# Kernel optimization log

Hardware: AMD Instinct MI355X
Metric: run time of the kernel (lower is better)

The kernel has to match this reference:

```python
import jax, jax.numpy as jnp
import numpy as np

B, IN_F, OUT_F = 1024, 512, 512


def setup_inputs() -> dict:
    key = jax.random.key(0)
    k1, k2 = jax.random.split(key)
    x = jax.random.uniform(k1, (B, IN_F), dtype=jnp.float32)
    weight = jax.random.uniform(k2, (IN_F, OUT_F), dtype=jnp.float32)
    return {"x": x, "weight": weight}


def reference(x, weight):
    # Max-min fuzzy composition (tropical semiring 'matmul'):
    # out[b, o] = max_i min(x[b, i], W[i, o])
    # x: [B, IN], weight: [IN, OUT] -> out: [B, OUT]
    return jnp.max(jnp.minimum(x[:, :, None], weight[None, :, :]), axis=1)
```

## Files before the change

kernel.cpp:

```cpp
#include <hip/hip_runtime.h>


typedef unsigned int u32;
typedef u32 u32x2 __attribute__((ext_vector_type(2)));
typedef u32 u32x4 __attribute__((ext_vector_type(4)));
typedef float f4 __attribute__((ext_vector_type(4)));
typedef float f2 __attribute__((ext_vector_type(2)));
typedef __fp16 h2 __attribute__((ext_vector_type(2)));

#define IN_F 512
#define OUT_F 512
#define XS_BYTES 8192
#define WS_BYTES 8192
#define BUF_BYTES (XS_BYTES + WS_BYTES)

static __device__ __forceinline__ u32 pkcvt(float a, float b) {
  return __builtin_bit_cast(u32, __builtin_amdgcn_cvt_pkrtz(a, b));
}
static __device__ __forceinline__ u32 pkmin(u32 a, u32 b) {
  u32 d;
  asm("v_pk_min_u16 %0, %1, %2" : "=v"(d) : "v"(a), "v"(b));
  return d;
}
static __device__ __forceinline__ u32 pkmax(u32 a, u32 b) {
  u32 d;
  asm("v_pk_max_u16 %0, %1, %2" : "=v"(d) : "v"(a), "v"(b));
  return d;
}

__global__ __launch_bounds__(1024, 4) void maxmin_v3(const float* __restrict__ X,
                                                     const float* __restrict__ W,
                                                     float* __restrict__ Out) {
  __shared__ __align__(16) char smem[65536];

  const int tid  = threadIdx.x;
  const int wv   = tid >> 6;
  const int lane = tid & 63;
  const int ty   = lane >> 3;
  const int tx   = lane & 7;
  const int b0   = blockIdx.x * 32;
  const int o0   = blockIdx.y * 64;

  const int xrow = tid & 31;
  const int xq   = tid >> 5;
  const bool dox = (xq < 16);
  const float* xg = X + (b0 + xrow) * IN_F + xq * 4;

  const int wrow = tid >> 4;
  const int wc4  = tid & 15;
  const float* wg = W + wrow * OUT_F + o0 + wc4 * 4;

  const int xs_r = (wv * 4) * 128 + ty * 16;
  const int ws_r = XS_BYTES + (wv * 4) * 128 + tx * 16;

  const int xw = xrow * 4;
  const int ww = XS_BYTES + wrow * 128 + wc4 * 8;

  u32 acc[4][4] = {};

  auto stage = [&](char* buf, f4 xv, f4 wv4) {
    u32x2 wp = {pkcvt(wv4.x, wv4.y), pkcvt(wv4.z, wv4.w)};
    *(u32x2*)(buf + ww) = wp;
    if (dox) {
      *(u32*)(buf + (4 * xq + 0) * 128 + xw) = pkcvt(xv.x, xv.x);
      *(u32*)(buf + (4 * xq + 1) * 128 + xw) = pkcvt(xv.y, xv.y);
      *(u32*)(buf + (4 * xq + 2) * 128 + xw) = pkcvt(xv.z, xv.z);
      *(u32*)(buf + (4 * xq + 3) * 128 + xw) = pkcvt(xv.w, xv.w);
    }
  };

  f4 xv = {};
  if (dox) xv = *(const f4*)xg;
  f4 wv4 = *(const f4*)wg;
  stage(smem, xv, wv4);
  __syncthreads();

  for (int c = 0; c < 8; ++c) {
    f4 nx = {}, nw = {};
    if (c < 7) {
      if (dox) nx = *(const f4*)(xg + (c + 1) * 64);
      nw = *(const f4*)(wg + (c + 1) * 64 * OUT_F);
    }
    const char* buf = smem + (c & 1) * BUF_BYTES;
#pragma unroll
    for (int j = 0; j < 4; ++j) {
      u32x4 xqv = *(const u32x4*)(buf + xs_r + j * 128);
      u32x4 wqv = *(const u32x4*)(buf + ws_r + j * 128);
#pragma unroll
      for (int i = 0; i < 4; ++i)
#pragma unroll
        for (int jj = 0; jj < 4; ++jj)
          acc[i][jj] = pkmax(acc[i][jj], pkmin(xqv[i], wqv[jj]));
    }
    if (c < 7) stage(smem + ((c + 1) & 1) * BUF_BYTES, nx, nw);
    __syncthreads();
  }

#pragma unroll
  for (int i = 0; i < 4; ++i) {
    u32x4 v = {acc[i][0], acc[i][1], acc[i][2], acc[i][3]};
    *(u32x4*)(smem + wv * 4096 + (4 * ty + i) * 128 + tx * 16) = v;
  }
  __syncthreads();

  const int row = tid >> 5;
  const int cp  = tid & 31;
  const int cb  = row * 128 + cp * 4;
  u32 m = *(const u32*)(smem + cb);
#pragma unroll
  for (int g = 1; g < 16; ++g) m = pkmax(m, *(const u32*)(smem + g * 4096 + cb));
  h2 hm = __builtin_bit_cast(h2, m);
  f2 o = {(float)hm.x, (float)hm.y};
  *(f2*)(Out + (b0 + row) * OUT_F + o0 + cp * 2) = o;
}

extern "C" void kernel_launch(void* const* d_in, const int* in_sizes, int n_in,
                              void* d_out, int out_size, void* d_ws, size_t ws_size,
                              hipStream_t stream) {
  const float* x = (const float*)d_in[0];
  const float* w = (const float*)d_in[1];
  float* out = (float*)d_out;
  (void)in_sizes; (void)n_in; (void)out_size; (void)d_ws; (void)ws_size;
  dim3 grid(1024 / 32, 512 / 64);
  maxmin_v3<<<grid, 1024, 0, stream>>>(x, w, out);
}
```

Baseline: 70.55 us.

## Pack x pairs along K and broadcast via op_sel with swizzled LDS layout

New measurement: 66.47 us. 1.06x faster.

```diff
diff --git a/kernel.cpp b/kernel.cpp
--- a/kernel.cpp
+++ b/kernel.cpp
@@ -8,27 +8,30 @@
 typedef float f2 __attribute__((ext_vector_type(2)));
 typedef __fp16 h2 __attribute__((ext_vector_type(2)));
 
-#define IN_F 512
-#define OUT_F 512
-#define XS_BYTES 8192
-#define WS_BYTES 8192
-#define BUF_BYTES (XS_BYTES + WS_BYTES)
+#define XB 8192
+#define WB 16384
+#define BUFB (XB + WB)
 
 static __device__ __forceinline__ u32 pkcvt(float a, float b) {
   return __builtin_bit_cast(u32, __builtin_amdgcn_cvt_pkrtz(a, b));
 }
-static __device__ __forceinline__ u32 pkmin(u32 a, u32 b) {
+static __device__ __forceinline__ u32 pkmax(u32 a, u32 b) {
+  u32 d; asm("v_pk_max_u16 %0, %1, %2" : "=v"(d) : "v"(a), "v"(b)); return d;
+}
+static __device__ __forceinline__ u32 pkmin_bl(u32 x, u32 w) {
   u32 d;
-  asm("v_pk_min_u16 %0, %1, %2" : "=v"(d) : "v"(a), "v"(b));
+  asm("v_pk_min_u16 %0, %1, %2 op_sel:[0,0] op_sel_hi:[0,1]"
+      : "=v"(d) : "v"(x), "v"(w));
   return d;
 }
-static __device__ __forceinline__ u32 pkmax(u32 a, u32 b) {
+static __device__ __forceinline__ u32 pkmin_bh(u32 x, u32 w) {
   u32 d;
-  asm("v_pk_max_u16 %0, %1, %2" : "=v"(d) : "v"(a), "v"(b));
+  asm("v_pk_min_u16 %0, %1, %2 op_sel:[1,0] op_sel_hi:[1,1]"
+      : "=v"(d) : "v"(x), "v"(w));
   return d;
 }
 
-__global__ __launch_bounds__(1024, 4) void maxmin_v3(const float* __restrict__ X,
+__global__ __launch_bounds__(1024, 4) void maxmin_v5(const float* __restrict__ X,
                                                      const float* __restrict__ W,
                                                      float* __restrict__ Out) {
   __shared__ __align__(16) char smem[65536];
@@ -41,65 +44,68 @@
   const int b0   = blockIdx.x * 32;
   const int o0   = blockIdx.y * 64;
 
-  const int xrow = tid & 31;
-  const int xq   = tid >> 5;
-  const bool dox = (xq < 16);
-  const float* xg = X + (b0 + xrow) * IN_F + xq * 4;
+  const int xr  = tid >> 5;
+  const int xkq = tid & 31;
+  const float* xg = X + (b0 + xr) * 512 + xkq * 4;
+  const int xw0 = (2 * xkq) * 128 + 4 * (xr ^ ((2 * xkq) & 28));
 
-  const int wrow = tid >> 4;
-  const int wc4  = tid & 15;
-  const float* wg = W + wrow * OUT_F + o0 + wc4 * 4;
+  const int wkk = tid >> 4;
+  const int wc4 = tid & 15;
+  const float* wg = W + wkk * 512 + o0 + wc4 * 4;
+  const int ww0 = XB + wkk * 128 + wc4 * 8;
 
-  const int xs_r = (wv * 4) * 128 + ty * 16;
-  const int ws_r = XS_BYTES + (wv * 4) * 128 + tx * 16;
-
-  const int xw = xrow * 4;
-  const int ww = XS_BYTES + wrow * 128 + wc4 * 8;
+  const int xro = 16 * (ty ^ (wv & 7));
+  const int wro = XB + 16 * tx;
 
   u32 acc[4][4] = {};
 
-  auto stage = [&](char* buf, f4 xv, f4 wv4) {
-    u32x2 wp = {pkcvt(wv4.x, wv4.y), pkcvt(wv4.z, wv4.w)};
-    *(u32x2*)(buf + ww) = wp;
-    if (dox) {
-      *(u32*)(buf + (4 * xq + 0) * 128 + xw) = pkcvt(xv.x, xv.x);
-      *(u32*)(buf + (4 * xq + 1) * 128 + xw) = pkcvt(xv.y, xv.y);
-      *(u32*)(buf + (4 * xq + 2) * 128 + xw) = pkcvt(xv.z, xv.z);
-      *(u32*)(buf + (4 * xq + 3) * 128 + xw) = pkcvt(xv.w, xv.w);
-    }
+  auto stage = [&](char* buf, f4 xv, f4 wa, f4 wb) {
+    *(u32*)(buf + xw0)       = pkcvt(xv.x, xv.y);
+    *(u32*)(buf + xw0 + 128) = pkcvt(xv.z, xv.w);
+    u32x2 wpa = {pkcvt(wa.x, wa.y), pkcvt(wa.z, wa.w)};
+    *(u32x2*)(buf + ww0) = wpa;
+    u32x2 wpb = {pkcvt(wb.x, wb.y), pkcvt(wb.z, wb.w)};
+    *(u32x2*)(buf + ww0 + 64 * 128) = wpb;
   };
 
-  f4 xv = {};
-  if (dox) xv = *(const f4*)xg;
-  f4 wv4 = *(const f4*)wg;
-  stage(smem, xv, wv4);
+  {
+    f4 xv = *(const f4*)xg;
+    f4 wa = *(const f4*)wg;
+    f4 wb = *(const f4*)(wg + 64 * 512);
+    stage(smem, xv, wa, wb);
+  }
   __syncthreads();
 
-  for (int c = 0; c < 8; ++c) {
-    f4 nx = {}, nw = {};
-    if (c < 7) {
-      if (dox) nx = *(const f4*)(xg + (c + 1) * 64);
-      nw = *(const f4*)(wg + (c + 1) * 64 * OUT_F);
+  for (int c = 0; c < 4; ++c) {
+    f4 nx = {}, na = {}, nb = {};
+    if (c < 3) {
+      nx = *(const f4*)(xg + (c + 1) * 128);
+      na = *(const f4*)(wg + (c + 1) * 128 * 512);
+      nb = *(const f4*)(wg + (c + 1) * 128 * 512 + 64 * 512);
     }
-    const char* buf = smem + (c & 1) * BUF_BYTES;
+    const char* buf = smem + (c & 1) * BUFB;
 #pragma unroll
-    for (int j = 0; j < 4; ++j) {
-      u32x4 xqv = *(const u32x4*)(buf + xs_r + j * 128);
-      u32x4 wqv = *(const u32x4*)(buf + ws_r + j * 128);
+    for (int q = 0; q < 4; ++q) {
+      const int kp = 4 * wv + q;
+      u32x4 xv = *(const u32x4*)(buf + kp * 128 + xro);
+      u32x4 wl = *(const u32x4*)(buf + wro + (2 * kp) * 128);
+      u32x4 wh = *(const u32x4*)(buf + wro + (2 * kp + 1) * 128);
 #pragma unroll
-      for (int i = 0; i < 4; ++i)
+      for (int j = 0; j < 4; ++j)
 #pragma unroll
-        for (int jj = 0; jj < 4; ++jj)
-          acc[i][jj] = pkmax(acc[i][jj], pkmin(xqv[i], wqv[jj]));
+        for (int cc = 0; cc < 4; ++cc) {
+          acc[j][cc] = pkmax(acc[j][cc], pkmin_bl(xv[j], wl[cc]));
+          acc[j][cc] = pkmax(acc[j][cc], pkmin_bh(xv[j], wh[cc]));
+        }
     }
-    if (c < 7) stage(smem + ((c + 1) & 1) * BUF_BYTES, nx, nw);
+    if (c < 3) stage(smem + ((c + 1) & 1) * BUFB, nx, na, nb);
     __syncthreads();
   }
 
 #pragma unroll
-  for (int i = 0; i < 4; ++i) {
-    u32x4 v = {acc[i][0], acc[i][1], acc[i][2], acc[i][3]};
-    *(u32x4*)(smem + wv * 4096 + (4 * ty + i) * 128 + tx * 16) = v;
+  for (int j = 0; j < 4; ++j) {
+    u32x4 v = {acc[j][0], acc[j][1], acc[j][2], acc[j][3]};
+    *(u32x4*)(smem + wv * 4096 + (4 * ty + j) * 128 + tx * 16) = v;
   }
   __syncthreads();
 
@@ -111,7 +117,7 @@
   for (int g = 1; g < 16; ++g) m = pkmax(m, *(const u32*)(smem + g * 4096 + cb));
   h2 hm = __builtin_bit_cast(h2, m);
   f2 o = {(float)hm.x, (float)hm.y};
-  *(f2*)(Out + (b0 + row) * OUT_F + o0 + cp * 2) = o;
+  *(f2*)(Out + (b0 + row) * 512 + o0 + cp * 2) = o;
 }
 
 extern "C" void kernel_launch(void* const* d_in, const int* in_sizes, int n_in,
@@ -122,5 +128,5 @@
   float* out = (float*)d_out;
   (void)in_sizes; (void)n_in; (void)out_size; (void)d_ws; (void)ws_size;
   dim3 grid(1024 / 32, 512 / 64);
-  maxmin_v3<<<grid, 1024, 0, stream>>>(x, w, out);
+  maxmin_v5<<<grid, 1024, 0, stream>>>(x, w, out);
 }
```
